# Performance work log

Hardware: AMD Instinct MI355X
Metric: run time of the kernel (lower is better)

Reference implementation:

```python
import jax, jax.numpy as jnp
import numpy as np

SLOPE = 0.2  # LeakyReLU negative slope

def _mlp2(x, w1, b1, w2, b2):
    h = jax.nn.leaky_relu(x @ w1 + b1, SLOPE)
    return h @ w2 + b2

def setup_inputs() -> dict:
    key = jax.random.key(0)
    ks = jax.random.split(key, 16)
    B, N, T, A, H = 8, 512, 8, 16, 64
    D = T * A  # node_dim * timestep = 128
    s = 0.1
    return {
        "nodes": jax.random.normal(ks[0], (B, N, T, A), dtype=jnp.float32),
        "edges": jax.random.randint(ks[1], (B, N, N), 0, 2),
        "self_w1": jax.random.normal(ks[2], (D, H), dtype=jnp.float32) * s,
        "self_b1": jnp.zeros((H,), jnp.float32),
        "self_w2": jax.random.normal(ks[3], (H, H), dtype=jnp.float32) * s,
        "self_b2": jnp.zeros((H,), jnp.float32),
        "nb_w1": jax.random.normal(ks[4], (D, H), dtype=jnp.float32) * s,
        "nb_b1": jnp.zeros((H,), jnp.float32),
        "nb_w2": jax.random.normal(ks[5], (H, H), dtype=jnp.float32) * s,
        "nb_b2": jnp.zeros((H,), jnp.float32),
        "comb_w1": jax.random.normal(ks[6], (2 * H, H), dtype=jnp.float32) * s,
        "comb_b1": jnp.zeros((H,), jnp.float32),
        "comb_w2": jax.random.normal(ks[7], (H, 1), dtype=jnp.float32) * s,
        "comb_b2": jnp.zeros((1,), jnp.float32),
    }

def reference(nodes, edges, self_w1, self_b1, self_w2, self_b2,
              nb_w1, nb_b1, nb_w2, nb_b2,
              comb_w1, comb_b1, comb_w2, comb_b2):
    B, N = nodes.shape[0], nodes.shape[1]
    H = self_w2.shape[1]
    x = nodes.reshape(B, N, -1)                       # [B,N,D]
    self_e = _mlp2(x, self_w1, self_b1, self_w2, self_b2)  # [B,N,H]
    nb_e = _mlp2(x, nb_w1, nb_b1, nb_w2, nb_b2)            # [B,N,H]

    # combine_mlp(cat(self_i, nb_j)) scores; split fc1 to avoid [B,N,N,2H]
    w1_s, w1_n = comb_w1[:H], comb_w1[H:]
    pre = (jnp.einsum('bih,hk->bik', self_e, w1_s)[:, :, None, :]
           + jnp.einsum('bjh,hk->bjk', nb_e, w1_n)[:, None, :, :]
           + comb_b1)                                  # [B,N,N,H] (i=target, j=neighbor)
    scores = (jax.nn.leaky_relu(pre, SLOPE) @ comb_w2)[..., 0] + comb_b2[0]  # [B,N,N]

    # mask[b,i,j] = edges[b,j,i] != 0 and i != j
    mask = (jnp.swapaxes(edges, 1, 2) != 0) & (~jnp.eye(N, dtype=bool))
    neg = jnp.finfo(scores.dtype).min
    weights = jax.nn.softmax(jnp.where(mask, scores, neg), axis=-1)
    weights = jnp.where(mask, weights, 0.0)

    agg = jnp.einsum('bij,bjh->bih', weights, nb_e)    # weighted neighbor sum
    has_nb = mask.any(-1)                              # nodes w/o neighbors stay zero
    return jnp.where(has_nb[..., None], agg + self_e, 0.0)
```

## Files before the change

kernel.cpp:

```cpp
#include <hip/hip_runtime.h>
#include <float.h>

typedef __attribute__((ext_vector_type(8))) short short8;
typedef __attribute__((ext_vector_type(4))) float f32x4;

#define SLOPE 0.2f

__device__ __forceinline__ float leaky(float x) { return fmaxf(x, SLOPE * x); }

__device__ __forceinline__ unsigned short f2bf(float f) {
  unsigned u = __float_as_uint(f);
  return (unsigned short)((u + 0x7FFFu + ((u >> 16) & 1u)) >> 16);
}

__global__ __launch_bounds__(256) void node_mlps(
    const float* __restrict__ nodes,
    const float* __restrict__ self_w1, const float* __restrict__ self_b1,
    const float* __restrict__ self_w2, const float* __restrict__ self_b2,
    const float* __restrict__ nb_w1,   const float* __restrict__ nb_b1,
    const float* __restrict__ nb_w2,   const float* __restrict__ nb_b2,
    const float* __restrict__ comb_w1, const float* __restrict__ comb_b1,
    const float* __restrict__ comb_w2, const float* __restrict__ comb_b2,
    float* __restrict__ self_e,
    float* __restrict__ ss, float* __restrict__ sn,
    float* __restrict__ sP, float* __restrict__ sQ,
    unsigned short* __restrict__ nbT)
{
  __shared__ float x_sh[8][128];
  __shared__ float h_sh[8][64];
  __shared__ float e_sh[8][64];

  const int tid = threadIdx.x, lane = tid & 63, wv = tid >> 6;
  const int node0 = blockIdx.x * 8;
  const int bb = node0 >> 9;
  const int jloc = node0 & 511;

  ((float4*)&x_sh[0][0])[tid] = ((const float4*)(nodes + (size_t)node0 * 128))[tid];
  __syncthreads();

  const int la = wv * 2, lb = la + 1;
  const float w2lane = comb_w2[lane];
  const float cb2 = comb_b2[0];
  const float cb1 = comb_b1[lane];

  for (int p = 0; p < 2; ++p) {
    const float* w1 = p ? nb_w1 : self_w1;
    const float* b1 = p ? nb_b1 : self_b1;
    const float* w2 = p ? nb_w2 : self_w2;
    const float* b2 = p ? nb_b2 : self_b2;
    const float* cw = comb_w1 + (p ? 64 * 64 : 0);

    float a0 = 0.f, a1 = 0.f, c0 = 0.f, c1 = 0.f;
    #pragma unroll 4
    for (int q = 0; q < 32; ++q) {
      float4 xa = *(const float4*)&x_sh[la][q * 4];
      float4 xb = *(const float4*)&x_sh[lb][q * 4];
      float w_0 = w1[(q * 4 + 0) * 64 + lane];
      float w_1 = w1[(q * 4 + 1) * 64 + lane];
      float w_2 = w1[(q * 4 + 2) * 64 + lane];
      float w_3 = w1[(q * 4 + 3) * 64 + lane];
      a0 += xa.x * w_0; a1 += xa.y * w_1; a0 += xa.z * w_2; a1 += xa.w * w_3;
      c0 += xb.x * w_0; c1 += xb.y * w_1; c0 += xb.z * w_2; c1 += xb.w * w_3;
    }
    {
      float bv = b1[lane];
      h_sh[la][lane] = leaky(a0 + a1 + bv);
      h_sh[lb][lane] = leaky(c0 + c1 + bv);
    }
    __syncthreads();

    a0 = a1 = c0 = c1 = 0.f;
    #pragma unroll 4
    for (int q = 0; q < 16; ++q) {
      float4 ha = *(const float4*)&h_sh[la][q * 4];
      float4 hb = *(const float4*)&h_sh[lb][q * 4];
      float w_0 = w2[(q * 4 + 0) * 64 + lane];
      float w_1 = w2[(q * 4 + 1) * 64 + lane];
      float w_2 = w2[(q * 4 + 2) * 64 + lane];
      float w_3 = w2[(q * 4 + 3) * 64 + lane];
      a0 += ha.x * w_0; a1 += ha.y * w_1; a0 += ha.z * w_2; a1 += ha.w * w_3;
      c0 += hb.x * w_0; c1 += hb.y * w_1; c0 += hb.z * w_2; c1 += hb.w * w_3;
    }
    float e_a, e_b;
    {
      float bv = b2[lane];
      e_a = a0 + a1 + bv;
      e_b = c0 + c1 + bv;
    }
    e_sh[la][lane] = e_a;
    e_sh[lb][lane] = e_b;
    if (p == 0) {
      self_e[(size_t)(node0 + la) * 64 + lane] = e_a;
      self_e[(size_t)(node0 + lb) * 64 + lane] = e_b;
    }
    __syncthreads();

    a0 = a1 = c0 = c1 = 0.f;
    #pragma unroll 4
    for (int q = 0; q < 16; ++q) {
      float4 ea = *(const float4*)&e_sh[la][q * 4];
      float4 eb = *(const float4*)&e_sh[lb][q * 4];
      float w_0 = cw[(q * 4 + 0) * 64 + lane];
      float w_1 = cw[(q * 4 + 1) * 64 + lane];
      float w_2 = cw[(q * 4 + 2) * 64 + lane];
      float w_3 = cw[(q * 4 + 3) * 64 + lane];
      a0 += ea.x * w_0; a1 += ea.y * w_1; a0 += ea.z * w_2; a1 += ea.w * w_3;
      c0 += eb.x * w_0; c1 += eb.y * w_1; c0 += eb.z * w_2; c1 += eb.w * w_3;
    }
    float s_a = a0 + a1 + (p ? 0.f : cb1);
    float s_b = c0 + c1 + (p ? 0.f : cb1);
    {
      float* so = p ? sn : ss;
      so[(size_t)(node0 + la) * 64 + lane] = s_a;
      so[(size_t)(node0 + lb) * 64 + lane] = s_b;
    }
    float ra = w2lane * s_a, rb = w2lane * s_b;
    #pragma unroll
    for (int off = 32; off; off >>= 1) {
      ra += __shfl_xor(ra, off);
      rb += __shfl_xor(rb, off);
    }
    if (lane == 0) {
      float* po = p ? sQ : sP;
      float add = p ? 0.f : cb2;
      po[node0 + la] = 0.6f * ra + add;
      po[node0 + lb] = 0.6f * rb + add;
    }

    if (p == 1) {
      float v0 = e_sh[la][lane];
      float v1 = e_sh[lb][lane];
      unsigned pack = (unsigned)f2bf(v0) | ((unsigned)f2bf(v1) << 16);
      unsigned* dst = (unsigned*)(nbT + ((size_t)(bb * 64 + lane) * 512 + jloc + la));
      *dst = pack;
    }
    __syncthreads();
  }
}

__global__ __launch_bounds__(512) void gat_attn(
    const int* __restrict__ edges,
    const float* __restrict__ comb_w2,
    const float* __restrict__ self_e,
    const float* __restrict__ ss, const float* __restrict__ sn,
    const float* __restrict__ sP, const float* __restrict__ sQ,
    const unsigned short* __restrict__ nbT,
    float* __restrict__ out)
{
  __shared__ __align__(16) float sn_sh[64][68];
  __shared__ __align__(16) float sc_f[16][520];
  __shared__ __align__(16) unsigned short sc_b[16][536];
  __shared__ __align__(16) unsigned short nbT_sh[64][520];
  __shared__ __align__(16) float red_sh[4][64][4];
  __shared__ float f_sh[16];

  const int tid = threadIdx.x, lane = tid & 63, wv = tid >> 6;
  const int blk = blockIdx.x;
  const int b = blk & 7, it = blk >> 3;
  const int i0 = it * 16;
  const size_t nodeb = (size_t)b * 512;

  const int ra = wv * 2, rb = ra + 1;
  const int ia = i0 + ra, ib = ia + 1;

  float4 w2p[16], sa0[16], sa1[16];
  {
    const float4* w2v = (const float4*)comb_w2;
    const float4* s0 = (const float4*)(ss + (nodeb + ia) * 64);
    const float4* s1 = (const float4*)(ss + (nodeb + ib) * 64);
    #pragma unroll
    for (int q = 0; q < 16; ++q) {
      float4 w = w2v[q];
      w2p[q] = make_float4(0.4f * w.x, 0.4f * w.y, 0.4f * w.z, 0.4f * w.w);
      sa0[q] = s0[q];
      sa1[q] = s1[q];
    }
  }
  const float sPa = sP[nodeb + ia], sPb = sP[nodeb + ib];

  for (int jt = 0; jt < 8; ++jt) {
    {
      const float4* src = (const float4*)(sn + (nodeb + jt * 64) * 64);
      for (int t = tid; t < 1024; t += 512) {
        int r = t >> 4, c = (t & 15) * 4;
        *(float4*)&sn_sh[r][c] = src[t];
      }
    }
    __syncthreads();

    const int j = jt * 64 + lane;
    const int2 ee = *(const int2*)&edges[((size_t)b * 512 + j) * 512 + ia];
    const float qj = sQ[nodeb + j];

    float acc0 = 0.f, acc1 = 0.f;
    #pragma unroll
    for (int q = 0; q < 16; ++q) {
      float4 v = *(const float4*)&sn_sh[lane][q * 4];
      float4 w = w2p[q];
      float4 A = sa0[q];
      float4 Bv = sa1[q];
      acc0 += w.x * fabsf(A.x + v.x) + w.y * fabsf(A.y + v.y)
            + w.z * fabsf(A.z + v.z) + w.w * fabsf(A.w + v.w);
      acc1 += w.x * fabsf(Bv.x + v.x) + w.y * fabsf(Bv.y + v.y)
            + w.z * fabsf(Bv.z + v.z) + w.w * fabsf(Bv.w + v.w);
    }
    sc_f[ra][j] = (ee.x != 0 && j != ia) ? acc0 + sPa + qj : -FLT_MAX;
    sc_f[rb][j] = (ee.y != 0 && j != ib) ? acc1 + sPb + qj : -FLT_MAX;
    __syncthreads();
  }

  float4 pa0 = *(const float4*)&sc_f[ra][lane * 8];
  float4 pa1 = *(const float4*)&sc_f[ra][lane * 8 + 4];
  float4 pb0 = *(const float4*)&sc_f[rb][lane * 8];
  float4 pb1 = *(const float4*)&sc_f[rb][lane * 8 + 4];

  float m0 = fmaxf(fmaxf(fmaxf(pa0.x, pa0.y), fmaxf(pa0.z, pa0.w)),
                   fmaxf(fmaxf(pa1.x, pa1.y), fmaxf(pa1.z, pa1.w)));
  float m1 = fmaxf(fmaxf(fmaxf(pb0.x, pb0.y), fmaxf(pb0.z, pb0.w)),
                   fmaxf(fmaxf(pb1.x, pb1.y), fmaxf(pb1.z, pb1.w)));
  #pragma unroll
  for (int off = 32; off; off >>= 1) {
    m0 = fmaxf(m0, __shfl_xor(m0, off));
    m1 = fmaxf(m1, __shfl_xor(m1, off));
  }

  pa0.x = __expf(pa0.x - m0); pa0.y = __expf(pa0.y - m0);
  pa0.z = __expf(pa0.z - m0); pa0.w = __expf(pa0.w - m0);
  pa1.x = __expf(pa1.x - m0); pa1.y = __expf(pa1.y - m0);
  pa1.z = __expf(pa1.z - m0); pa1.w = __expf(pa1.w - m0);
  pb0.x = __expf(pb0.x - m1); pb0.y = __expf(pb0.y - m1);
  pb0.z = __expf(pb0.z - m1); pb0.w = __expf(pb0.w - m1);
  pb1.x = __expf(pb1.x - m1); pb1.y = __expf(pb1.y - m1);
  pb1.z = __expf(pb1.z - m1); pb1.w = __expf(pb1.w - m1);

  float s0 = pa0.x + pa0.y + pa0.z + pa0.w + pa1.x + pa1.y + pa1.z + pa1.w;
  float s1 = pb0.x + pb0.y + pb0.z + pb0.w + pb1.x + pb1.y + pb1.z + pb1.w;
  #pragma unroll
  for (int off = 32; off; off >>= 1) {
    s0 += __shfl_xor(s0, off);
    s1 += __shfl_xor(s1, off);
  }

  {
    uint4 wa, wb;
    wa.x = (unsigned)f2bf(pa0.x) | ((unsigned)f2bf(pa0.y) << 16);
    wa.y = (unsigned)f2bf(pa0.z) | ((unsigned)f2bf(pa0.w) << 16);
    wa.z = (unsigned)f2bf(pa1.x) | ((unsigned)f2bf(pa1.y) << 16);
    wa.w = (unsigned)f2bf(pa1.z) | ((unsigned)f2bf(pa1.w) << 16);
    wb.x = (unsigned)f2bf(pb0.x) | ((unsigned)f2bf(pb0.y) << 16);
    wb.y = (unsigned)f2bf(pb0.z) | ((unsigned)f2bf(pb0.w) << 16);
    wb.z = (unsigned)f2bf(pb1.x) | ((unsigned)f2bf(pb1.y) << 16);
    wb.w = (unsigned)f2bf(pb1.z) | ((unsigned)f2bf(pb1.w) << 16);
    *(uint4*)&sc_b[ra][lane * 8] = wa;
    *(uint4*)&sc_b[rb][lane * 8] = wb;
  }
  if (lane == 0) {
    f_sh[ra] = (m0 > -1e37f) ? 1.0f / s0 : 0.0f;
    f_sh[rb] = (m1 > -1e37f) ? 1.0f / s1 : 0.0f;
  }
  __syncthreads();

  {
    const short8* src = (const short8*)(nbT + (size_t)b * 64 * 512);
    for (int t = tid; t < 4096; t += 512) {
      int r = t >> 6, c = (t & 63) * 8;
      *(short8*)&nbT_sh[r][c] = src[t];
    }
  }
  __syncthreads();

  const int nt = wv & 3, kh = wv >> 2;
  const int arow = lane & 15, agrp = lane >> 4;
  const int bcol = nt * 16 + (lane & 15);

  f32x4 C = {0.f, 0.f, 0.f, 0.f};
  #pragma unroll
  for (int ks = 0; ks < 8; ++ks) {
    const int jb = kh * 256 + ks * 32 + agrp * 8;
    short8 afr = *(const short8*)&sc_b[arow][jb];
    short8 bfr = *(const short8*)&nbT_sh[bcol][jb];
    C = __builtin_amdgcn_mfma_f32_16x16x32_bf16(afr, bfr, C, 0, 0, 0);
  }
  if (kh == 1) *(f32x4*)&red_sh[wv - 4][lane][0] = C;
  __syncthreads();
  if (kh == 0) {
    f32x4 P = *(const f32x4*)&red_sh[wv][lane][0];
    #pragma unroll
    for (int r = 0; r < 4; ++r) {
      const int rg = agrp * 4 + r;
      const float f = f_sh[rg];
      const size_t adr = (nodeb + i0 + rg) * 64 + bcol;
      const float val = (C[r] + P[r]) * f + self_e[adr];
      out[adr] = (f > 0.f) ? val : 0.f;
    }
  }
}

extern "C" void kernel_launch(void* const* d_in, const int* in_sizes, int n_in,
                              void* d_out, int out_size, void* d_ws, size_t ws_size,
                              hipStream_t stream) {
  const float* nodes   = (const float*)d_in[0];
  const int*   edges   = (const int*)  d_in[1];
  const float* self_w1 = (const float*)d_in[2];
  const float* self_b1 = (const float*)d_in[3];
  const float* self_w2 = (const float*)d_in[4];
  const float* self_b2 = (const float*)d_in[5];
  const float* nb_w1   = (const float*)d_in[6];
  const float* nb_b1   = (const float*)d_in[7];
  const float* nb_w2   = (const float*)d_in[8];
  const float* nb_b2   = (const float*)d_in[9];
  const float* comb_w1 = (const float*)d_in[10];
  const float* comb_b1 = (const float*)d_in[11];
  const float* comb_w2 = (const float*)d_in[12];
  const float* comb_b2 = (const float*)d_in[13];

  float* ws     = (float*)d_ws;
  float* self_e = ws;
  float* ss     = ws + 262144;
  float* sn     = ws + 524288;
  float* sP     = ws + 786432;
  float* sQ     = ws + 790528;
  unsigned short* nbT = (unsigned short*)(ws + 794624);

  node_mlps<<<512, 256, 0, stream>>>(
      nodes, self_w1, self_b1, self_w2, self_b2,
      nb_w1, nb_b1, nb_w2, nb_b2, comb_w1, comb_b1, comb_w2, comb_b2,
      self_e, ss, sn, sP, sQ, nbT);

  gat_attn<<<256, 512, 0, stream>>>(
      edges, comb_w2, self_e, ss, sn, sP, sQ, nbT, (float*)d_out);
}
```

Baseline: 35.84 us.

## Restructure attention scoring so each thread owns a neighbor column with transposed sn

The neighbor projection sn is now written transposed (snT), and in the attention kernel each thread owns one neighbor j, holding its 64-element sn vector and 64 scaled weights in registers while looping over the 16 target rows. Edges are read as contiguous int4 rows and packed into a 16-bit mask. Softmax max and sum are reduced across waves through small shared arrays. This removes the 8-iteration shared-memory staging loop, its barriers and the fp32 score buffer, at the cost of heavy register use (about 128+ floats per thread), which risks spills or lower occupancy.

```diff
diff --git a/kernel.cpp b/kernel.cpp
--- a/kernel.cpp
+++ b/kernel.cpp
@@ -22,7 +22,7 @@
     const float* __restrict__ comb_w1, const float* __restrict__ comb_b1,
     const float* __restrict__ comb_w2, const float* __restrict__ comb_b2,
     float* __restrict__ self_e,
-    float* __restrict__ ss, float* __restrict__ sn,
+    float* __restrict__ ss, float* __restrict__ snT,
     float* __restrict__ sP, float* __restrict__ sQ,
     unsigned short* __restrict__ nbT)
 {
@@ -109,10 +109,12 @@
     }
     float s_a = a0 + a1 + (p ? 0.f : cb1);
     float s_b = c0 + c1 + (p ? 0.f : cb1);
-    {
-      float* so = p ? sn : ss;
-      so[(size_t)(node0 + la) * 64 + lane] = s_a;
-      so[(size_t)(node0 + lb) * 64 + lane] = s_b;
+    if (p == 0) {
+      ss[(size_t)(node0 + la) * 64 + lane] = s_a;
+      ss[(size_t)(node0 + lb) * 64 + lane] = s_b;
+    } else {
+      *(float2*)(snT + ((size_t)(bb * 64 + lane)) * 512 + jloc + la) =
+          make_float2(s_a, s_b);
     }
     float ra = w2lane * s_a, rb = w2lane * s_b;
     #pragma unroll
@@ -131,8 +133,7 @@
       float v0 = e_sh[la][lane];
       float v1 = e_sh[lb][lane];
       unsigned pack = (unsigned)f2bf(v0) | ((unsigned)f2bf(v1) << 16);
-      unsigned* dst = (unsigned*)(nbT + ((size_t)(bb * 64 + lane) * 512 + jloc + la));
-      *dst = pack;
+      *(unsigned*)(nbT + ((size_t)(bb * 64 + lane) * 512 + jloc + la)) = pack;
     }
     __syncthreads();
   }
@@ -142,16 +143,17 @@
     const int* __restrict__ edges,
     const float* __restrict__ comb_w2,
     const float* __restrict__ self_e,
-    const float* __restrict__ ss, const float* __restrict__ sn,
+    const float* __restrict__ ss, const float* __restrict__ snT,
     const float* __restrict__ sP, const float* __restrict__ sQ,
     const unsigned short* __restrict__ nbT,
     float* __restrict__ out)
 {
-  __shared__ __align__(16) float sn_sh[64][68];
-  __shared__ __align__(16) float sc_f[16][520];
-  __shared__ __align__(16) unsigned short sc_b[16][536];
+  __shared__ __align__(16) unsigned short P_sh[16][520];
   __shared__ __align__(16) unsigned short nbT_sh[64][520];
   __shared__ __align__(16) float red_sh[4][64][4];
+  __shared__ float rmax_sh[8][16];
+  __shared__ float rsum_sh[8][16];
+  __shared__ float mx_sh[16];
   __shared__ float f_sh[16];
 
   const int tid = threadIdx.x, lane = tid & 63, wv = tid >> 6;
@@ -159,115 +161,90 @@
   const int b = blk & 7, it = blk >> 3;
   const int i0 = it * 16;
   const size_t nodeb = (size_t)b * 512;
-
-  const int ra = wv * 2, rb = ra + 1;
-  const int ia = i0 + ra, ib = ia + 1;
-
-  float4 w2p[16], sa0[16], sa1[16];
+  const int j = wv * 64 + lane;
+
+  #pragma unroll
+  for (int r8 = 0; r8 < 8; ++r8) {
+    const int r = wv * 8 + r8;
+    short8 v = *(const short8*)(nbT + ((size_t)(b * 64 + r)) * 512 + lane * 8);
+    *(short8*)&nbT_sh[r][lane * 8] = v;
+  }
+
+  float snv[64];
+  #pragma unroll
+  for (int k = 0; k < 64; ++k)
+    snv[k] = snT[((size_t)(b * 64 + k)) * 512 + j];
+
+  float w2p[64];
+  #pragma unroll
+  for (int k = 0; k < 64; ++k) w2p[k] = 0.4f * comb_w2[k];
+
+  const float sQj = sQ[nodeb + j];
+
+  unsigned emask = 0;
   {
-    const float4* w2v = (const float4*)comb_w2;
-    const float4* s0 = (const float4*)(ss + (nodeb + ia) * 64);
-    const float4* s1 = (const float4*)(ss + (nodeb + ib) * 64);
+    const int* er = edges + ((size_t)(nodeb + j)) * 512 + i0;
+    #pragma unroll
+    for (int c = 0; c < 4; ++c) {
+      int4 e4 = *(const int4*)(er + c * 4);
+      emask |= (e4.x != 0 ? 1u : 0u) << (c * 4 + 0);
+      emask |= (e4.y != 0 ? 1u : 0u) << (c * 4 + 1);
+      emask |= (e4.z != 0 ? 1u : 0u) << (c * 4 + 2);
+      emask |= (e4.w != 0 ? 1u : 0u) << (c * 4 + 3);
+    }
+    const int d = j - i0;
+    if (d >= 0 && d < 16) emask &= ~(1u << d);
+  }
+
+  float msc[16];
+  #pragma unroll
+  for (int i = 0; i < 16; ++i) {
+    const float4* srow = (const float4*)(ss + (nodeb + i0 + i) * 64);
+    float a0 = 0.f, a1 = 0.f;
     #pragma unroll
     for (int q = 0; q < 16; ++q) {
-      float4 w = w2v[q];
-      w2p[q] = make_float4(0.4f * w.x, 0.4f * w.y, 0.4f * w.z, 0.4f * w.w);
-      sa0[q] = s0[q];
-      sa1[q] = s1[q];
-    }
-  }
-  const float sPa = sP[nodeb + ia], sPb = sP[nodeb + ib];
-
-  for (int jt = 0; jt < 8; ++jt) {
-    {
-      const float4* src = (const float4*)(sn + (nodeb + jt * 64) * 64);
-      for (int t = tid; t < 1024; t += 512) {
-        int r = t >> 4, c = (t & 15) * 4;
-        *(float4*)&sn_sh[r][c] = src[t];
-      }
-    }
-    __syncthreads();
-
-    const int j = jt * 64 + lane;
-    const int2 ee = *(const int2*)&edges[((size_t)b * 512 + j) * 512 + ia];
-    const float qj = sQ[nodeb + j];
-
-    float acc0 = 0.f, acc1 = 0.f;
-    #pragma unroll
-    for (int q = 0; q < 16; ++q) {
-      float4 v = *(const float4*)&sn_sh[lane][q * 4];
-      float4 w = w2p[q];
-      float4 A = sa0[q];
-      float4 Bv = sa1[q];
-      acc0 += w.x * fabsf(A.x + v.x) + w.y * fabsf(A.y + v.y)
-            + w.z * fabsf(A.z + v.z) + w.w * fabsf(A.w + v.w);
-      acc1 += w.x * fabsf(Bv.x + v.x) + w.y * fabsf(Bv.y + v.y)
-            + w.z * fabsf(Bv.z + v.z) + w.w * fabsf(Bv.w + v.w);
-    }
-    sc_f[ra][j] = (ee.x != 0 && j != ia) ? acc0 + sPa + qj : -FLT_MAX;
-    sc_f[rb][j] = (ee.y != 0 && j != ib) ? acc1 + sPb + qj : -FLT_MAX;
-    __syncthreads();
-  }
-
-  float4 pa0 = *(const float4*)&sc_f[ra][lane * 8];
-  float4 pa1 = *(const float4*)&sc_f[ra][lane * 8 + 4];
-  float4 pb0 = *(const float4*)&sc_f[rb][lane * 8];
-  float4 pb1 = *(const float4*)&sc_f[rb][lane * 8 + 4];
-
-  float m0 = fmaxf(fmaxf(fmaxf(pa0.x, pa0.y), fmaxf(pa0.z, pa0.w)),
-                   fmaxf(fmaxf(pa1.x, pa1.y), fmaxf(pa1.z, pa1.w)));
-  float m1 = fmaxf(fmaxf(fmaxf(pb0.x, pb0.y), fmaxf(pb0.z, pb0.w)),
-                   fmaxf(fmaxf(pb1.x, pb1.y), fmaxf(pb1.z, pb1.w)));
-  #pragma unroll
-  for (int off = 32; off; off >>= 1) {
-    m0 = fmaxf(m0, __shfl_xor(m0, off));
-    m1 = fmaxf(m1, __shfl_xor(m1, off));
-  }
-
-  pa0.x = __expf(pa0.x - m0); pa0.y = __expf(pa0.y - m0);
-  pa0.z = __expf(pa0.z - m0); pa0.w = __expf(pa0.w - m0);
-  pa1.x = __expf(pa1.x - m0); pa1.y = __expf(pa1.y - m0);
-  pa1.z = __expf(pa1.z - m0); pa1.w = __expf(pa1.w - m0);
-  pb0.x = __expf(pb0.x - m1); pb0.y = __expf(pb0.y - m1);
-  pb0.z = __expf(pb0.z - m1); pb0.w = __expf(pb0.w - m1);
-  pb1.x = __expf(pb1.x - m1); pb1.y = __expf(pb1.y - m1);
-  pb1.z = __expf(pb1.z - m1); pb1.w = __expf(pb1.w - m1);
-
-  float s0 = pa0.x + pa0.y + pa0.z + pa0.w + pa1.x + pa1.y + pa1.z + pa1.w;
-  float s1 = pb0.x + pb0.y + pb0.z + pb0.w + pb1.x + pb1.y + pb1.z + pb1.w;
-  #pragma unroll
-  for (int off = 32; off; off >>= 1) {
-    s0 += __shfl_xor(s0, off);
-    s1 += __shfl_xor(s1, off);
-  }
-
-  {
-    uint4 wa, wb;
-    wa.x = (unsigned)f2bf(pa0.x) | ((unsigned)f2bf(pa0.y) << 16);
-    wa.y = (unsigned)f2bf(pa0.z) | ((unsigned)f2bf(pa0.w) << 16);
-    wa.z = (unsigned)f2bf(pa1.x) | ((unsigned)f2bf(pa1.y) << 16);
-    wa.w = (unsigned)f2bf(pa1.z) | ((unsigned)f2bf(pa1.w) << 16);
-    wb.x = (unsigned)f2bf(pb0.x) | ((unsigned)f2bf(pb0.y) << 16);
-    wb.y = (unsigned)f2bf(pb0.z) | ((unsigned)f2bf(pb0.w) << 16);
-    wb.z = (unsigned)f2bf(pb1.x) | ((unsigned)f2bf(pb1.y) << 16);
-    wb.w = (unsigned)f2bf(pb1.z) | ((unsigned)f2bf(pb1.w) << 16);
-    *(uint4*)&sc_b[ra][lane * 8] = wa;
-    *(uint4*)&sc_b[rb][lane * 8] = wb;
-  }
-  if (lane == 0) {
-    f_sh[ra] = (m0 > -1e37f) ? 1.0f / s0 : 0.0f;
-    f_sh[rb] = (m1 > -1e37f) ? 1.0f / s1 : 0.0f;
-  }
-  __syncthreads();
-
-  {
-    const short8* src = (const short8*)(nbT + (size_t)b * 64 * 512);
-    for (int t = tid; t < 4096; t += 512) {
-      int r = t >> 6, c = (t & 63) * 8;
-      *(short8*)&nbT_sh[r][c] = src[t];
-    }
-  }
-  __syncthreads();
+      float4 s4 = srow[q];
+      a0 += w2p[q * 4 + 0] * fabsf(s4.x + snv[q * 4 + 0]);
+      a1 += w2p[q * 4 + 1] * fabsf(s4.y + snv[q * 4 + 1]);
+      a0 += w2p[q * 4 + 2] * fabsf(s4.z + snv[q * 4 + 2]);
+      a1 += w2p[q * 4 + 3] * fabsf(s4.w + snv[q * 4 + 3]);
+    }
+    const float sc = a0 + a1 + sP[nodeb + i0 + i] + sQj;
+    msc[i] = ((emask >> i) & 1u) ? sc : -FLT_MAX;
+  }
+
+  #pragma unroll
+  for (int i = 0; i < 16; ++i) {
+    float v = msc[i];
+    #pragma unroll
+    for (int off = 32; off; off >>= 1) v = fmaxf(v, __shfl_xor(v, off));
+    if (lane == 0) rmax_sh[wv][i] = v;
+  }
+  __syncthreads();
+  if (tid < 16) {
+    float m = rmax_sh[0][tid];
+    #pragma unroll
+    for (int w = 1; w < 8; ++w) m = fmaxf(m, rmax_sh[w][tid]);
+    mx_sh[tid] = m;
+  }
+  __syncthreads();
+
+  #pragma unroll
+  for (int i = 0; i < 16; ++i) {
+    const float e = __expf(msc[i] - mx_sh[i]);
+    P_sh[i][j] = f2bf(e);
+    float v = e;
+    #pragma unroll
+    for (int off = 32; off; off >>= 1) v += __shfl_xor(v, off);
+    if (lane == 0) rsum_sh[wv][i] = v;
+  }
+  __syncthreads();
+  if (tid < 16) {
+    float s = rsum_sh[0][tid];
+    #pragma unroll
+    for (int w = 1; w < 8; ++w) s += rsum_sh[w][tid];
+    f_sh[tid] = (mx_sh[tid] > -1e37f) ? 1.0f / s : 0.0f;
+  }
 
   const int nt = wv & 3, kh = wv >> 2;
   const int arow = lane & 15, agrp = lane >> 4;
@@ -277,7 +254,7 @@
   #pragma unroll
   for (int ks = 0; ks < 8; ++ks) {
     const int jb = kh * 256 + ks * 32 + agrp * 8;
-    short8 afr = *(const short8*)&sc_b[arow][jb];
+    short8 afr = *(const short8*)&P_sh[arow][jb];
     short8 bfr = *(const short8*)&nbT_sh[bcol][jb];
     C = __builtin_amdgcn_mfma_f32_16x16x32_bf16(afr, bfr, C, 0, 0, 0);
   }
@@ -317,7 +294,7 @@
   float* ws     = (float*)d_ws;
   float* self_e = ws;
   float* ss     = ws + 262144;
-  float* sn     = ws + 524288;
+  float* snT    = ws + 524288;
   float* sP     = ws + 786432;
   float* sQ     = ws + 790528;
   unsigned short* nbT = (unsigned short*)(ws + 794624);
@@ -325,8 +302,8 @@
   node_mlps<<<512, 256, 0, stream>>>(
       nodes, self_w1, self_b1, self_w2, self_b2,
       nb_w1, nb_b1, nb_w2, nb_b2, comb_w1, comb_b1, comb_w2, comb_b2,
-      self_e, ss, sn, sP, sQ, nbT);
+      self_e, ss, snT, sP, sQ, nbT);
 
   gat_attn<<<256, 512, 0, stream>>>(
-      edges, comb_w2, self_e, ss, sn, sP, sQ, nbT, (float*)d_out);
+      edges, comb_w2, self_e, ss, snT, sP, sQ, nbT, (float*)d_out);
 }
```

New measurement: 42.21 us. 17.8% more time.

## Double-buffer neighbor tiles, keep scores in registers, read nbT from global

Applied to the files above, without the earlier changes.

The attention kernel now prefetches the next sn tile into registers and double-buffers it in shared memory, which removes one barrier per tile. Edge masks and sQ values are hoisted into a bitmask and a register array before the loop. Scores stay in registers for the softmax instead of going through shared memory, and the MFMA B operand is read straight from global nbT rather than staged in LDS. Together these cut LDS traffic, LDS footprint and barriers, in exchange for more register pressure and uncoalesced-ish global loads in the MFMA loop.

```diff
diff --git a/kernel.cpp b/kernel.cpp
--- a/kernel.cpp
+++ b/kernel.cpp
@@ -131,8 +131,7 @@
       float v0 = e_sh[la][lane];
       float v1 = e_sh[lb][lane];
       unsigned pack = (unsigned)f2bf(v0) | ((unsigned)f2bf(v1) << 16);
-      unsigned* dst = (unsigned*)(nbT + ((size_t)(bb * 64 + lane) * 512 + jloc + la));
-      *dst = pack;
+      *(unsigned*)(nbT + ((size_t)(bb * 64 + lane) * 512 + jloc + la)) = pack;
     }
     __syncthreads();
   }
@@ -147,21 +146,35 @@
     const unsigned short* __restrict__ nbT,
     float* __restrict__ out)
 {
-  __shared__ __align__(16) float sn_sh[64][68];
-  __shared__ __align__(16) float sc_f[16][520];
-  __shared__ __align__(16) unsigned short sc_b[16][536];
-  __shared__ __align__(16) unsigned short nbT_sh[64][520];
+  __shared__ __align__(16) float sn_sh[2][64][68];
+  __shared__ __align__(16) unsigned short P_sh[16][520];
   __shared__ __align__(16) float red_sh[4][64][4];
   __shared__ float f_sh[16];
 
   const int tid = threadIdx.x, lane = tid & 63, wv = tid >> 6;
-  const int blk = blockIdx.x;
-  const int b = blk & 7, it = blk >> 3;
+  const int b = blockIdx.x & 7, it = blockIdx.x >> 3;
   const int i0 = it * 16;
   const size_t nodeb = (size_t)b * 512;
 
   const int ra = wv * 2, rb = ra + 1;
   const int ia = i0 + ra, ib = ia + 1;
+
+  unsigned em0 = 0, em1 = 0;
+  float sQv[8];
+  #pragma unroll
+  for (int jt = 0; jt < 8; ++jt) {
+    const int j = jt * 64 + lane;
+    int2 e2 = *(const int2*)&edges[((size_t)(nodeb + j)) * 512 + ia];
+    sQv[jt] = sQ[nodeb + j];
+    em0 |= (e2.x != 0 ? 1u : 0u) << jt;
+    em1 |= (e2.y != 0 ? 1u : 0u) << jt;
+  }
+  {
+    const int d0 = ia - lane;
+    if (d0 >= 0 && (d0 & 63) == 0) em0 &= ~(1u << (d0 >> 6));
+    const int d1 = ib - lane;
+    if (d1 >= 0 && (d1 & 63) == 0) em1 &= ~(1u << (d1 >> 6));
+  }
 
   float4 w2p[16], sa0[16], sa1[16];
   {
@@ -178,24 +191,31 @@
   }
   const float sPa = sP[nodeb + ia], sPb = sP[nodeb + ib];
 
+  const int str = tid >> 4, stc = (tid & 15) * 4;
+  const int str2 = (tid + 512) >> 4, stc2 = ((tid + 512) & 15) * 4;
+  float4 st0, st1;
+  {
+    const float4* src = (const float4*)(sn + nodeb * 64);
+    st0 = src[tid];
+    st1 = src[tid + 512];
+  }
+
+  float msc0[8], msc1[8];
+  int cur = 0;
   for (int jt = 0; jt < 8; ++jt) {
-    {
-      const float4* src = (const float4*)(sn + (nodeb + jt * 64) * 64);
-      for (int t = tid; t < 1024; t += 512) {
-        int r = t >> 4, c = (t & 15) * 4;
-        *(float4*)&sn_sh[r][c] = src[t];
-      }
+    *(float4*)&sn_sh[cur][str][stc] = st0;
+    *(float4*)&sn_sh[cur][str2][stc2] = st1;
+    if (jt < 7) {
+      const float4* src = (const float4*)(sn + (nodeb + (jt + 1) * 64) * 64);
+      st0 = src[tid];
+      st1 = src[tid + 512];
     }
     __syncthreads();
-
-    const int j = jt * 64 + lane;
-    const int2 ee = *(const int2*)&edges[((size_t)b * 512 + j) * 512 + ia];
-    const float qj = sQ[nodeb + j];
 
     float acc0 = 0.f, acc1 = 0.f;
     #pragma unroll
     for (int q = 0; q < 16; ++q) {
-      float4 v = *(const float4*)&sn_sh[lane][q * 4];
+      float4 v = *(const float4*)&sn_sh[cur][lane][q * 4];
       float4 w = w2p[q];
       float4 A = sa0[q];
       float4 Bv = sa1[q];
@@ -204,81 +224,55 @@
       acc1 += w.x * fabsf(Bv.x + v.x) + w.y * fabsf(Bv.y + v.y)
             + w.z * fabsf(Bv.z + v.z) + w.w * fabsf(Bv.w + v.w);
     }
-    sc_f[ra][j] = (ee.x != 0 && j != ia) ? acc0 + sPa + qj : -FLT_MAX;
-    sc_f[rb][j] = (ee.y != 0 && j != ib) ? acc1 + sPb + qj : -FLT_MAX;
-    __syncthreads();
-  }
-
-  float4 pa0 = *(const float4*)&sc_f[ra][lane * 8];
-  float4 pa1 = *(const float4*)&sc_f[ra][lane * 8 + 4];
-  float4 pb0 = *(const float4*)&sc_f[rb][lane * 8];
-  float4 pb1 = *(const float4*)&sc_f[rb][lane * 8 + 4];
-
-  float m0 = fmaxf(fmaxf(fmaxf(pa0.x, pa0.y), fmaxf(pa0.z, pa0.w)),
-                   fmaxf(fmaxf(pa1.x, pa1.y), fmaxf(pa1.z, pa1.w)));
-  float m1 = fmaxf(fmaxf(fmaxf(pb0.x, pb0.y), fmaxf(pb0.z, pb0.w)),
-                   fmaxf(fmaxf(pb1.x, pb1.y), fmaxf(pb1.z, pb1.w)));
+    msc0[jt] = ((em0 >> jt) & 1u) ? acc0 + sPa + sQv[jt] : -FLT_MAX;
+    msc1[jt] = ((em1 >> jt) & 1u) ? acc1 + sPb + sQv[jt] : -FLT_MAX;
+    cur ^= 1;
+  }
+
+  float m0 = msc0[0], m1 = msc1[0];
+  #pragma unroll
+  for (int jt = 1; jt < 8; ++jt) {
+    m0 = fmaxf(m0, msc0[jt]);
+    m1 = fmaxf(m1, msc1[jt]);
+  }
   #pragma unroll
   for (int off = 32; off; off >>= 1) {
     m0 = fmaxf(m0, __shfl_xor(m0, off));
     m1 = fmaxf(m1, __shfl_xor(m1, off));
   }
 
-  pa0.x = __expf(pa0.x - m0); pa0.y = __expf(pa0.y - m0);
-  pa0.z = __expf(pa0.z - m0); pa0.w = __expf(pa0.w - m0);
-  pa1.x = __expf(pa1.x - m0); pa1.y = __expf(pa1.y - m0);
-  pa1.z = __expf(pa1.z - m0); pa1.w = __expf(pa1.w - m0);
-  pb0.x = __expf(pb0.x - m1); pb0.y = __expf(pb0.y - m1);
-  pb0.z = __expf(pb0.z - m1); pb0.w = __expf(pb0.w - m1);
-  pb1.x = __expf(pb1.x - m1); pb1.y = __expf(pb1.y - m1);
-  pb1.z = __expf(pb1.z - m1); pb1.w = __expf(pb1.w - m1);
-
-  float s0 = pa0.x + pa0.y + pa0.z + pa0.w + pa1.x + pa1.y + pa1.z + pa1.w;
-  float s1 = pb0.x + pb0.y + pb0.z + pb0.w + pb1.x + pb1.y + pb1.z + pb1.w;
+  float s0 = 0.f, s1 = 0.f;
+  #pragma unroll
+  for (int jt = 0; jt < 8; ++jt) {
+    const float e0 = __expf(msc0[jt] - m0);
+    const float e1 = __expf(msc1[jt] - m1);
+    P_sh[ra][jt * 64 + lane] = f2bf(e0);
+    P_sh[rb][jt * 64 + lane] = f2bf(e1);
+    s0 += e0;
+    s1 += e1;
+  }
   #pragma unroll
   for (int off = 32; off; off >>= 1) {
     s0 += __shfl_xor(s0, off);
     s1 += __shfl_xor(s1, off);
   }
-
-  {
-    uint4 wa, wb;
-    wa.x = (unsigned)f2bf(pa0.x) | ((unsigned)f2bf(pa0.y) << 16);
-    wa.y = (unsigned)f2bf(pa0.z) | ((unsigned)f2bf(pa0.w) << 16);
-    wa.z = (unsigned)f2bf(pa1.x) | ((unsigned)f2bf(pa1.y) << 16);
-    wa.w = (unsigned)f2bf(pa1.z) | ((unsigned)f2bf(pa1.w) << 16);
-    wb.x = (unsigned)f2bf(pb0.x) | ((unsigned)f2bf(pb0.y) << 16);
-    wb.y = (unsigned)f2bf(pb0.z) | ((unsigned)f2bf(pb0.w) << 16);
-    wb.z = (unsigned)f2bf(pb1.x) | ((unsigned)f2bf(pb1.y) << 16);
-    wb.w = (unsigned)f2bf(pb1.z) | ((unsigned)f2bf(pb1.w) << 16);
-    *(uint4*)&sc_b[ra][lane * 8] = wa;
-    *(uint4*)&sc_b[rb][lane * 8] = wb;
-  }
   if (lane == 0) {
     f_sh[ra] = (m0 > -1e37f) ? 1.0f / s0 : 0.0f;
     f_sh[rb] = (m1 > -1e37f) ? 1.0f / s1 : 0.0f;
   }
   __syncthreads();
 
-  {
-    const short8* src = (const short8*)(nbT + (size_t)b * 64 * 512);
-    for (int t = tid; t < 4096; t += 512) {
-      int r = t >> 6, c = (t & 63) * 8;
-      *(short8*)&nbT_sh[r][c] = src[t];
-    }
-  }
-  __syncthreads();
-
   const int nt = wv & 3, kh = wv >> 2;
   const int arow = lane & 15, agrp = lane >> 4;
   const int bcol = nt * 16 + (lane & 15);
+  const unsigned short* nbrow = nbT + ((size_t)(b * 64 + bcol)) * 512;
 
   f32x4 C = {0.f, 0.f, 0.f, 0.f};
   #pragma unroll
   for (int ks = 0; ks < 8; ++ks) {
     const int jb = kh * 256 + ks * 32 + agrp * 8;
-    short8 afr = *(const short8*)&sc_b[arow][jb];
-    short8 bfr = *(const short8*)&nbT_sh[bcol][jb];
+    short8 afr = *(const short8*)&P_sh[arow][jb];
+    short8 bfr = *(const short8*)(nbrow + jb);
     C = __builtin_amdgcn_mfma_f32_16x16x32_bf16(afr, bfr, C, 0, 0, 0);
   }
   if (kh == 1) *(f32x4*)&red_sh[wv - 4][lane][0] = C;
```

Result: slower. 38.86 us (+8.4%).
